# Performance work log

Measured on AMD Instinct MI355X. Metric: run time of the kernel, lower is better.

Reference implementation:

```python
import jax, jax.numpy as jnp
import numpy as np


def _segsum(x):
    """Stable segment-sum. x: (..., l) -> (..., l, l) lower-triangular sums."""
    l = x.shape[-1]
    cs = jnp.cumsum(x, axis=-1)
    seg = cs[..., :, None] - cs[..., None, :]
    mask = jnp.tril(jnp.ones((l, l), dtype=bool))
    return jnp.where(mask, seg, -jnp.inf)


def setup_inputs() -> dict:
    key = jax.random.key(0)
    kx, ka, kb, kc = jax.random.split(key, 4)
    b, s, h, p, n = 4, 8192, 32, 64, 16
    X = jax.random.normal(kx, (b, s, h, p), dtype=jnp.float32)
    # negative A for realistic decaying SSM dynamics / numerical safety
    A = -jnp.abs(jax.random.normal(ka, (b, s, h), dtype=jnp.float32)) * 0.5
    B = jax.random.normal(kb, (b, s, h, n), dtype=jnp.float32)
    C = jax.random.normal(kc, (b, s, h, n), dtype=jnp.float32)
    return {"X": X, "A": A, "B": B, "C": C, "block_len": 64}


def reference(X, A, B, C, block_len):
    b, s, h, p = X.shape
    n = B.shape[-1]
    c = s // block_len
    l = block_len
    # chunk: (b, c, l, ...)
    Xb = X.reshape(b, c, l, h, p)
    Bb = B.reshape(b, c, l, h, n)
    Cb = C.reshape(b, c, l, h, n)
    Ab = A.reshape(b, c, l, h).transpose(0, 3, 1, 2)  # (b, h, c, l)
    A_cumsum = jnp.cumsum(Ab, axis=-1)                # (b, h, c, l)

    # 1) intra-chunk (diagonal) output
    L = jnp.exp(_segsum(Ab))                          # (b, h, c, l, l)
    Y_diag = jnp.einsum("bclhn,bcshn,bhcls,bcshp->bclhp", Cb, Bb, L, Xb)

    # 2) intra-chunk states (chunk-final state contribution)
    decay_states = jnp.exp(A_cumsum[..., -1:] - A_cumsum)   # (b, h, c, l)
    states = jnp.einsum("bclhn,bhcl,bclhp->bchpn", Bb, decay_states, Xb)

    # 3) inter-chunk recurrence (zero initial states)
    A_last = A_cumsum[..., -1]                        # (b, h, c)
    decay_chunk = jnp.exp(_segsum(jnp.pad(A_last, ((0, 0), (0, 0), (1, 0)))))  # (b,h,c+1,c+1)
    states = jnp.concatenate([jnp.zeros_like(states[:, :1]), states], axis=1)  # (b,c+1,h,p,n)
    new_states = jnp.einsum("bhzc,bchpn->bzhpn", decay_chunk, states)
    states = new_states[:, :-1]                       # states entering each chunk

    # 4) state -> output (off-diagonal)
    state_decay_out = jnp.exp(A_cumsum)               # (b, h, c, l)
    Y_off = jnp.einsum("bclhn,bchpn,bhcl->bclhp", Cb, states, state_decay_out)

    Y = (Y_diag + Y_off).reshape(b, s, h, p)
    return Y
```

## Files before the change

kernel.cpp:

```cpp
#include <hip/hip_runtime.h>

#define BB 4
#define SS 8192
#define HH 32
#define PP 64
#define NN 16
#define LL 64
#define CC 128
#define NCHAIN (BB * HH)
#define NCHT (NCHAIN * CC)
#define ITERS 8
#define GRID1 (NCHT / ITERS)

typedef __attribute__((ext_vector_type(8))) short bf16x8;
typedef __attribute__((ext_vector_type(4))) short s16x4;
typedef __attribute__((ext_vector_type(4))) float f32x4;

#define LBAR() do { \
    __builtin_amdgcn_sched_barrier(0); \
    asm volatile("s_waitcnt lgkmcnt(0)" ::: "memory"); \
    __builtin_amdgcn_s_barrier(); \
    __builtin_amdgcn_sched_barrier(0); \
} while (0)

__device__ inline short f2bf(float f) {
    unsigned u = __builtin_bit_cast(unsigned, f);
    u = (u + 0x7FFFu + ((u >> 16) & 1u)) >> 16;
    return (short)u;
}
__device__ inline float bf2f(short s) {
    unsigned u = ((unsigned)(unsigned short)s) << 16;
    return __builtin_bit_cast(float, u);
}
__device__ inline float wscan(float v, int l) {
    float x = v;
#pragma unroll
    for (int d = 1; d < 64; d <<= 1) {
        float t = __shfl_up(x, d, 64);
        if (l >= d) x += t;
    }
    return x;
}

__global__ __launch_bounds__(256) void k1_states(
    const float* __restrict__ X, const float* __restrict__ A,
    const float* __restrict__ B, short* __restrict__ states,
    float* __restrict__ alast_g, short* __restrict__ xtf, int do_xtf)
{
    int tid = threadIdx.x;
    int w = tid >> 6, l = tid & 63, g = l >> 4, lr = l & 15;
    int r = tid >> 2, q4 = tid & 3;
    int bid = blockIdx.x;

    __shared__ float Bs[2][LL][17];

    float xrA[16], xrB[16];
    float4 br; float av;

#define K1_LOADS(gc_, xr_) { \
    int h_ = (gc_) & 31, c_ = ((gc_) >> 5) & 127, b_ = (gc_) >> 12; \
    size_t row0_ = (size_t)b_ * SS + (size_t)c_ * LL; \
    const float* Xp_ = X + (row0_ * HH + h_) * PP; \
    av = (A + row0_ * HH + h_)[(size_t)l * HH]; \
    br = *(const float4*)(B + (row0_ * HH + h_) * NN + (size_t)r * (HH * NN) + q4 * 4); \
    _Pragma("unroll") for (int kt_ = 0; kt_ < 2; ++kt_) \
    _Pragma("unroll") for (int e_ = 0; e_ < 8; ++e_) \
        xr_[kt_ * 8 + e_] = Xp_[(size_t)(kt_ * 32 + g * 8 + e_) * (HH * PP) + 16 * w + lr]; }

#define K1_STAGE(qd_, gc_) { \
    float x_ = wscan(av, l); \
    float alast_ = __shfl(x_, 63, 64); \
    float wlr_ = __expf(alast_ - __shfl(x_, r, 64)); \
    Bs[qd_][r][q4 * 4 + 0] = br.x * wlr_; \
    Bs[qd_][r][q4 * 4 + 1] = br.y * wlr_; \
    Bs[qd_][r][q4 * 4 + 2] = br.z * wlr_; \
    Bs[qd_][r][q4 * 4 + 3] = br.w * wlr_; \
    if (tid == 0) { \
        int h_ = (gc_) & 31, c_ = ((gc_) >> 5) & 127, b_ = (gc_) >> 12; \
        alast_g[(b_ * HH + h_) * CC + c_] = alast_; } }

#define K1_COMPUTE(qd_, xr_, gc_) { \
    int h_ = (gc_) & 31, c_ = ((gc_) >> 5) & 127, b_ = (gc_) >> 12; \
    size_t cc_ = (size_t)((b_ * HH + h_) * CC + c_); \
    bf16x8 bt0_, bt1_, xf0_, xf1_; \
    _Pragma("unroll") for (int e_ = 0; e_ < 8; ++e_) { \
        bt0_[e_] = f2bf(Bs[qd_][g * 8 + e_][lr]); \
        bt1_[e_] = f2bf(Bs[qd_][32 + g * 8 + e_][lr]); \
        xf0_[e_] = f2bf(xr_[e_]); xf1_[e_] = f2bf(xr_[8 + e_]); } \
    f32x4 st_ = __builtin_amdgcn_mfma_f32_16x16x32_bf16(bt0_, xf0_, (f32x4)0.f, 0, 0, 0); \
    st_ = __builtin_amdgcn_mfma_f32_16x16x32_bf16(bt1_, xf1_, st_, 0, 0, 0); \
    s16x4 sp_ = { f2bf(st_[0]), f2bf(st_[1]), f2bf(st_[2]), f2bf(st_[3]) }; \
    *(s16x4*)(states + (cc_ << 10) + ((16 * w + lr) << 4) + (g << 2)) = sp_; \
    if (do_xtf) { \
        short* xd_ = xtf + (cc_ << 12); \
        ((bf16x8*)xd_)[tid] = xf0_; \
        ((bf16x8*)xd_)[tid + 256] = xf1_; } }

    K1_LOADS(bid, xrA)
    K1_STAGE(0, bid)
    LBAR();
#pragma unroll
    for (int t = 0; t < ITERS; ++t) {
        int gc_c = bid + t * GRID1;
        int gc_n = bid + (t + 1) * GRID1;
        if (t + 1 < ITERS) {
            if (t & 1) { K1_LOADS(gc_n, xrA) } else { K1_LOADS(gc_n, xrB) }
        }
        if (t & 1) { K1_COMPUTE(t & 1, xrB, gc_c) } else { K1_COMPUTE(t & 1, xrA, gc_c) }
        if (t + 1 < ITERS) {
            K1_STAGE((t & 1) ^ 1, gc_n)
            LBAR();
        }
    }
#undef K1_LOADS
#undef K1_STAGE
#undef K1_COMPUTE
}

__global__ __launch_bounds__(256) void k2_scan(
    short* __restrict__ states, const float* __restrict__ alast_g)
{
    int chain = blockIdx.x >> 2;
    int t = ((blockIdx.x & 3) << 8) + threadIdx.x;
    __shared__ float eal[CC];
    if (threadIdx.x < CC)
        eal[threadIdx.x] = __expf(alast_g[chain * CC + threadIdx.x]);
    __syncthreads();

    short* base = states + ((size_t)chain * CC << 10) + t;
    float P = 0.f;
    for (int c0 = 0; c0 < CC; c0 += 8) {
        short s[8];
#pragma unroll
        for (int u = 0; u < 8; ++u) s[u] = base[(size_t)(c0 + u) << 10];
#pragma unroll
        for (int u = 0; u < 8; ++u) {
            float o = P;
            P = eal[c0 + u] * P + bf2f(s[u]);
            base[(size_t)(c0 + u) << 10] = f2bf(o);
        }
    }
}

__global__ __launch_bounds__(256) void k3_big(
    const float* __restrict__ A, const float* __restrict__ Bm,
    const float* __restrict__ Cm, const short* __restrict__ pin,
    const short* __restrict__ xtf, float* __restrict__ Y)
{
    int tid = threadIdx.x;
    int w = tid >> 6, l = tid & 63, g = l >> 4, lr = l & 15;
    int r = tid >> 2, q4 = tid & 3;
    int bid = blockIdx.x;

    __shared__ short ScF[8 * 64 * 8];
    __shared__ short BsF[2][4 * 64 * 8];
    __shared__ short CsF[2][4 * 64 * 8];
    __shared__ short PF [2][4 * 64 * 8];

    ((bf16x8*)ScF)[tid] = (bf16x8)0;
    ((bf16x8*)ScF)[tid + 256] = (bf16x8)0;
    if (tid < 128) {
        int zs = (tid >> 5) * 64 + 32 + (tid & 31);
        ((bf16x8*)BsF[0])[zs] = (bf16x8)0;  ((bf16x8*)BsF[1])[zs] = (bf16x8)0;
        ((bf16x8*)CsF[0])[zs] = (bf16x8)0;  ((bf16x8*)CsF[1])[zs] = (bf16x8)0;
        ((bf16x8*)PF [0])[zs] = (bf16x8)0;  ((bf16x8*)PF [1])[zs] = (bf16x8)0;
    }

    bf16x8 xv0n, xv1n, xv0c, xv1c;
    float4 br, cr0 = {0,0,0,0}, cr1 = {0,0,0,0};
    s16x4 pinb; float av;
    float x_c, x_n;

#define K3_LOADS(gc_) { \
    int h_ = (gc_) & 31, c_ = ((gc_) >> 5) & 127, b_ = (gc_) >> 12; \
    size_t row0_ = (size_t)b_ * SS + (size_t)c_ * LL; \
    size_t cc_ = (size_t)((b_ * HH + h_) * CC + c_); \
    const short* xs_ = xtf + (cc_ << 12); \
    xv0n = ((const bf16x8*)xs_)[tid]; \
    xv1n = ((const bf16x8*)xs_)[tid + 256]; \
    av = (A + row0_ * HH + h_)[(size_t)l * HH]; \
    br = *(const float4*)(Bm + (row0_ * HH + h_) * NN + (size_t)r * (HH * NN) + q4 * 4); \
    if (g < 2) { \
        const float* cp_ = Cm + (row0_ * HH + h_) * NN + (size_t)(16 * w + lr) * (HH * NN) + g * 8; \
        cr0 = *(const float4*)cp_; cr1 = *(const float4*)(cp_ + 4); } \
    pinb = *(const s16x4*)(pin + (cc_ << 10) + ((16 * w + lr) << 4) + (g << 2)); }

#define K3_STAGE(qd_) { \
    x_n = wscan(av, l); \
    int fl_ = (r & 15) + 16 * (q4 >> 1); \
    int jt_ = r >> 4; \
    s16x4 bb_ = { f2bf(br.x), f2bf(br.y), f2bf(br.z), f2bf(br.w) }; \
    ((s16x4*)BsF[qd_])[(jt_ * 64 + fl_) * 2 + (q4 & 1)] = bb_; \
    ((s16x4*)PF[qd_])[(w * 64 + (g >> 1) * 16 + lr) * 2 + (g & 1)] = pinb; \
    if (g < 2) { \
        bf16x8 cw_; \
        cw_[0]=f2bf(cr0.x); cw_[1]=f2bf(cr0.y); cw_[2]=f2bf(cr0.z); cw_[3]=f2bf(cr0.w); \
        cw_[4]=f2bf(cr1.x); cw_[5]=f2bf(cr1.y); cw_[6]=f2bf(cr1.z); cw_[7]=f2bf(cr1.w); \
        ((bf16x8*)CsF[qd_])[w * 64 + g * 16 + lr] = cw_; } }

#define SCORE_TILE(IT, JT, MASK) { \
    bf16x8 ca_ = ((bf16x8*)CsF[qb])[(IT) * 64 + l]; \
    bf16x8 bw_ = ((bf16x8*)BsF[qb])[(JT) * 64 + l]; \
    f32x4 sr_ = __builtin_amdgcn_mfma_f32_16x16x32_bf16(ca_, bw_, (f32x4)0.f, 0, 0, 0); \
    float csj_ = __shfl(x_c, (JT) * 16 + lr, 64); \
    float enj_ = __expf(-csj_); \
    _Pragma("unroll") for (int rr = 0; rr < 4; ++rr) { \
        float v_ = sr_[rr] * (eii[IT][rr] * enj_); \
        if (MASK) v_ = ((JT) * 16 + lr <= (IT) * 16 + 4 * g + rr) ? v_ : 0.f; \
        ScF[(((IT) * 2 + ((JT) >> 1)) * 64 + ((2 * (JT) + (lr >> 3)) & 3) * 16 + 4 * g + rr) * 8 + (lr & 7)] = f2bf(v_); } }

    K3_LOADS(bid)
    K3_STAGE(0)
    x_c = x_n; xv0c = xv0n; xv1c = xv1n;
    LBAR();

#pragma unroll 2
    for (int t = 0; t < ITERS; ++t) {
        int gc = bid + t * GRID1;
        int qb = t & 1;
        if (t + 1 < ITERS) { K3_LOADS(bid + (t + 1) * GRID1) }

        float eii[4][4];
#pragma unroll
        for (int it = 0; it < 4; ++it)
#pragma unroll
            for (int rr = 0; rr < 4; ++rr)
                eii[it][rr] = __expf(__shfl(x_c, 16 * it + 4 * g + rr, 64));

        f32x4 acc[4];
        {
            bf16x8 pfw = ((bf16x8*)PF[qb])[w * 64 + l];
#pragma unroll
            for (int it = 0; it < 4; ++it) {
                bf16x8 ca = ((bf16x8*)CsF[qb])[it * 64 + l];
                acc[it] = __builtin_amdgcn_mfma_f32_16x16x32_bf16(ca, pfw, (f32x4)0.f, 0, 0, 0);
            }
#pragma unroll
            for (int it = 0; it < 4; ++it)
#pragma unroll
                for (int rr = 0; rr < 4; ++rr) acc[it][rr] *= eii[it][rr];
        }

        if (w == 0)      { SCORE_TILE(0,0,true)  SCORE_TILE(2,1,false) SCORE_TILE(3,2,false) }
        else if (w == 1) { SCORE_TILE(1,0,false) SCORE_TILE(2,2,true)  SCORE_TILE(3,3,true)  }
        else if (w == 2) { SCORE_TILE(1,1,true)  SCORE_TILE(3,0,false) }
        else             { SCORE_TILE(2,0,false) SCORE_TILE(3,1,false) }

        LBAR();

#pragma unroll
        for (int it = 0; it < 4; ++it) {
            bf16x8 af0 = ((bf16x8*)ScF)[(it * 2 + 0) * 64 + l];
            acc[it] = __builtin_amdgcn_mfma_f32_16x16x32_bf16(af0, xv0c, acc[it], 0, 0, 0);
        }
#pragma unroll
        for (int it = 2; it < 4; ++it) {
            bf16x8 af1 = ((bf16x8*)ScF)[(it * 2 + 1) * 64 + l];
            acc[it] = __builtin_amdgcn_mfma_f32_16x16x32_bf16(af1, xv1c, acc[it], 0, 0, 0);
        }
        {
            int h_ = gc & 31, c_ = (gc >> 5) & 127, b_ = gc >> 12;
            size_t row0_ = (size_t)b_ * SS + (size_t)c_ * LL;
            float* Yp = Y + (row0_ * HH + h_) * PP;
#pragma unroll
            for (int it = 0; it < 4; ++it)
#pragma unroll
                for (int rr = 0; rr < 4; ++rr)
                    Yp[(size_t)(16 * it + 4 * g + rr) * (HH * PP) + 16 * w + lr] = acc[it][rr];
        }

        if (t + 1 < ITERS) { K3_STAGE((t + 1) & 1) }
        LBAR();
        x_c = x_n; xv0c = xv0n; xv1c = xv1n;
    }
#undef K3_LOADS
#undef K3_STAGE
#undef SCORE_TILE
}

__global__ __launch_bounds__(256) void k3_small(
    const float* __restrict__ X, const float* __restrict__ A,
    const float* __restrict__ Bm, const float* __restrict__ Cm,
    const short* __restrict__ pin, float* __restrict__ Y)
{
    int blk = blockIdx.x;
    int h = blk & (HH - 1);
    int c = (blk >> 5) & (CC - 1);
    int b = blk >> 12;
    int tid = threadIdx.x;
    int w = tid >> 6, l = tid & 63, g = l >> 4, lr = l & 15;
    int chain = b * HH + h;
    int r = tid >> 2, q = tid & 3;

    __shared__ short XTF[8 * 64 * 8];
    __shared__ short ScF[8 * 64 * 8];
    __shared__ short BsF[4 * 64 * 8];
    __shared__ short PF[4 * 64 * 8];

    size_t row0 = (size_t)b * SS + (size_t)c * LL;
    const float* Xp = X + (row0 * HH + h) * PP;
    const float* Bp = Bm + (row0 * HH + h) * NN;
    const float* Cp = Cm + (row0 * HH + h) * NN;
    const float* Ap = A + row0 * HH + h;
    float* Yp = Y + (row0 * HH + h) * PP;

    float av = Ap[(size_t)l * HH];
    float4 br = *(const float4*)(Bp + (size_t)r * (HH * NN) + q * 4);
    float4 cr0 = {0,0,0,0}, cr1 = {0,0,0,0};
    if (g < 2) {
        const float* crp = Cp + (size_t)(16 * w + lr) * (HH * NN) + g * 8;
        cr0 = *(const float4*)crp;
        cr1 = *(const float4*)(crp + 4);
    }
    s16x4 pinb = *(const s16x4*)(pin + (((size_t)(chain * CC + c)) << 10) + ((16 * w + lr) << 4) + (g << 2));
    float xr[16];
#pragma unroll
    for (int si = 0; si < 2; ++si)
#pragma unroll
        for (int e = 0; e < 8; ++e)
            xr[si * 8 + e] = Xp[(size_t)(si * 32 + g * 8 + e) * (HH * PP) + 16 * w + lr];

    float x = wscan(av, l);

    ((bf16x8*)ScF)[w * 128 + l] = (bf16x8)0;
    ((bf16x8*)ScF)[w * 128 + 64 + l] = (bf16x8)0;
    if (tid < 128)
        ((bf16x8*)PF)[(tid >> 5) * 64 + 32 + (tid & 31)] = (bf16x8)0;
    {
        int zt = tid >> 6, zu = (tid >> 1) & 31, zv = tid & 1;
        ((s16x4*)BsF)[(zt * 64 + 32 + zu) * 2 + zv] = (s16x4)0;
    }
    {
        int fl = (r & 15) + 16 * (q >> 1);
        int jt = r >> 4;
        s16x4 bb = { f2bf(br.x), f2bf(br.y), f2bf(br.z), f2bf(br.w) };
        ((s16x4*)BsF)[(jt * 64 + fl) * 2 + (q & 1)] = bb;
    }
    *(s16x4*)&PF[(w * 64 + (g >> 1) * 16 + lr) * 8 + (g & 1) * 4] = pinb;
    bf16x8 caw = (bf16x8)0;
    if (g < 2) {
        caw[0] = f2bf(cr0.x); caw[1] = f2bf(cr0.y);
        caw[2] = f2bf(cr0.z); caw[3] = f2bf(cr0.w);
        caw[4] = f2bf(cr1.x); caw[5] = f2bf(cr1.y);
        caw[6] = f2bf(cr1.z); caw[7] = f2bf(cr1.w);
    }
    __syncthreads();

    float cs_i[4], ei[4];
    int ib = 16 * w + 4 * g;
#pragma unroll
    for (int rr = 0; rr < 4; ++rr) {
        cs_i[rr] = __shfl(x, ib + rr, 64);
        ei[rr] = __expf(cs_i[rr]);
    }

    f32x4 acc[4];
#pragma unroll
    for (int pt = 0; pt < 4; ++pt) {
        bf16x8 pfv = ((bf16x8*)PF)[pt * 64 + l];
        acc[pt] = __builtin_amdgcn_mfma_f32_16x16x32_bf16(caw, pfv, (f32x4)0.f, 0, 0, 0);
    }
#pragma unroll
    for (int pt = 0; pt < 4; ++pt)
#pragma unroll
        for (int rr = 0; rr < 4; ++rr) acc[pt][rr] *= ei[rr];

    for (int jt = 0; jt <= w; ++jt) {
        bf16x8 bw = ((bf16x8*)BsF)[jt * 64 + l];
        f32x4 sr = __builtin_amdgcn_mfma_f32_16x16x32_bf16(caw, bw, (f32x4)0.f, 0, 0, 0);
        int j = jt * 16 + lr;
        float csj = __shfl(x, j, 64);
        int kt2 = j >> 5;
        int flb = 16 * ((j >> 3) & 3);
#pragma unroll
        for (int rr = 0; rr < 4; ++rr) {
            int i15 = g * 4 + rr;
            int i = 16 * w + i15;
            float v = (j <= i) ? sr[rr] * __expf(cs_i[rr] - csj) : 0.f;
            ScF[((w * 2 + kt2) * 64 + i15 + flb) * 8 + (j & 7)] = f2bf(v);
        }
    }

#pragma unroll
    for (int si = 0; si < 2; ++si) {
        bf16x8 xb;
#pragma unroll
        for (int e = 0; e < 8; ++e) xb[e] = f2bf(xr[si * 8 + e]);
        ((bf16x8*)XTF)[tid + si * 256] = xb;
    }
    __syncthreads();

    int kts = (w >= 2) ? 2 : 1;
    for (int kt = 0; kt < kts; ++kt) {
        bf16x8 af = ((bf16x8*)ScF)[(w * 2 + kt) * 64 + l];
#pragma unroll
        for (int pt = 0; pt < 4; ++pt) {
            bf16x8 xf = ((bf16x8*)XTF)[(kt * 4 + pt) * 64 + l];
            acc[pt] = __builtin_amdgcn_mfma_f32_16x16x32_bf16(af, xf, acc[pt], 0, 0, 0);
        }
    }

#pragma unroll
    for (int pt = 0; pt < 4; ++pt)
#pragma unroll
        for (int rr = 0; rr < 4; ++rr)
            Yp[(size_t)(16 * w + 4 * g + rr) * (HH * PP) + pt * 16 + lr] = acc[pt][rr];
}

extern "C" void kernel_launch(void* const* d_in, const int* in_sizes, int n_in,
                              void* d_out, int out_size, void* d_ws, size_t ws_size,
                              hipStream_t stream)
{
    const float* X = (const float*)d_in[0];
    const float* A = (const float*)d_in[1];
    const float* B = (const float*)d_in[2];
    const float* C = (const float*)d_in[3];
    float* Y = (float*)d_out;

    const size_t states_bytes = (size_t)NCHT * 1024 * 2;
    const size_t alast_bytes  = (size_t)NCHT * 4;
    const size_t xtf_bytes    = (size_t)NCHT * 4096 * 2;
    short* states = (short*)d_ws;
    float* alast  = (float*)((char*)d_ws + states_bytes);
    short* xtf    = (short*)((char*)d_ws + states_bytes + alast_bytes);
    int big = (ws_size >= states_bytes + alast_bytes + xtf_bytes) ? 1 : 0;

    dim3 blk(256);
    k1_states<<<dim3(GRID1), blk, 0, stream>>>(X, A, B, states, alast, xtf, big);
    k2_scan<<<dim3(NCHAIN * 4), blk, 0, stream>>>(states, alast);
    if (big)
        k3_big<<<dim3(GRID1), blk, 0, stream>>>(A, B, C, states, xtf, Y);
    else
        k3_small<<<dim3(NCHT), blk, 0, stream>>>(X, A, B, C, states, Y);
}
```

Before: 257.6 us.

## Vectorize scan to paired bf16, coalesce C loads, hoist exps, add setprio

The scan kernel now handles two bf16 state elements per thread via 32-bit accesses and launches half as many blocks. In k3, C is loaded by every thread with the same coalesced float4 pattern as B, replacing the half-wave 8-wide loads. Exponentials are computed once per lane and broadcast by shuffle instead of being recomputed per tile, and s_setprio is raised around the MFMA sections. The cost is less parallelism in the scan and a changed C LDS layout that must still match the SCORE_TILE reads.

```diff
diff --git a/kernel.cpp b/kernel.cpp
--- a/kernel.cpp
+++ b/kernel.cpp
@@ -120,24 +120,29 @@
 __global__ __launch_bounds__(256) void k2_scan(
     short* __restrict__ states, const float* __restrict__ alast_g)
 {
-    int chain = blockIdx.x >> 2;
-    int t = ((blockIdx.x & 3) << 8) + threadIdx.x;
+    int chain = blockIdx.x >> 1;
+    int t2 = ((blockIdx.x & 1) << 8) + threadIdx.x;
     __shared__ float eal[CC];
     if (threadIdx.x < CC)
         eal[threadIdx.x] = __expf(alast_g[chain * CC + threadIdx.x]);
     __syncthreads();
 
-    short* base = states + ((size_t)chain * CC << 10) + t;
-    float P = 0.f;
+    unsigned* base = (unsigned*)(states + ((size_t)chain * CC << 10)) + t2;
+    float P0 = 0.f, P1 = 0.f;
     for (int c0 = 0; c0 < CC; c0 += 8) {
-        short s[8];
-#pragma unroll
-        for (int u = 0; u < 8; ++u) s[u] = base[(size_t)(c0 + u) << 10];
+        unsigned s[8];
+#pragma unroll
+        for (int u = 0; u < 8; ++u) s[u] = base[(size_t)(c0 + u) << 9];
 #pragma unroll
         for (int u = 0; u < 8; ++u) {
-            float o = P;
-            P = eal[c0 + u] * P + bf2f(s[u]);
-            base[(size_t)(c0 + u) << 10] = f2bf(o);
+            float e = eal[c0 + u];
+            float f0 = bf2f((short)(s[u] & 0xFFFFu));
+            float f1 = bf2f((short)(s[u] >> 16));
+            unsigned o = (unsigned)(unsigned short)f2bf(P0)
+                       | ((unsigned)(unsigned short)f2bf(P1) << 16);
+            P0 = e * P0 + f0;
+            P1 = e * P1 + f1;
+            base[(size_t)(c0 + u) << 9] = o;
         }
     }
 }
@@ -167,7 +172,7 @@
     }
 
     bf16x8 xv0n, xv1n, xv0c, xv1c;
-    float4 br, cr0 = {0,0,0,0}, cr1 = {0,0,0,0};
+    float4 br, crv;
     s16x4 pinb; float av;
     float x_c, x_n;
 
@@ -180,9 +185,7 @@
     xv1n = ((const bf16x8*)xs_)[tid + 256]; \
     av = (A + row0_ * HH + h_)[(size_t)l * HH]; \
     br = *(const float4*)(Bm + (row0_ * HH + h_) * NN + (size_t)r * (HH * NN) + q4 * 4); \
-    if (g < 2) { \
-        const float* cp_ = Cm + (row0_ * HH + h_) * NN + (size_t)(16 * w + lr) * (HH * NN) + g * 8; \
-        cr0 = *(const float4*)cp_; cr1 = *(const float4*)(cp_ + 4); } \
+    crv = *(const float4*)(Cm + (row0_ * HH + h_) * NN + (size_t)r * (HH * NN) + q4 * 4); \
     pinb = *(const s16x4*)(pin + (cc_ << 10) + ((16 * w + lr) << 4) + (g << 2)); }
 
 #define K3_STAGE(qd_) { \
@@ -191,19 +194,15 @@
     int jt_ = r >> 4; \
     s16x4 bb_ = { f2bf(br.x), f2bf(br.y), f2bf(br.z), f2bf(br.w) }; \
     ((s16x4*)BsF[qd_])[(jt_ * 64 + fl_) * 2 + (q4 & 1)] = bb_; \
-    ((s16x4*)PF[qd_])[(w * 64 + (g >> 1) * 16 + lr) * 2 + (g & 1)] = pinb; \
-    if (g < 2) { \
-        bf16x8 cw_; \
-        cw_[0]=f2bf(cr0.x); cw_[1]=f2bf(cr0.y); cw_[2]=f2bf(cr0.z); cw_[3]=f2bf(cr0.w); \
-        cw_[4]=f2bf(cr1.x); cw_[5]=f2bf(cr1.y); cw_[6]=f2bf(cr1.z); cw_[7]=f2bf(cr1.w); \
-        ((bf16x8*)CsF[qd_])[w * 64 + g * 16 + lr] = cw_; } }
+    s16x4 cc_ = { f2bf(crv.x), f2bf(crv.y), f2bf(crv.z), f2bf(crv.w) }; \
+    ((s16x4*)CsF[qd_])[(jt_ * 64 + fl_) * 2 + (q4 & 1)] = cc_; \
+    ((s16x4*)PF[qd_])[(w * 64 + (g >> 1) * 16 + lr) * 2 + (g & 1)] = pinb; }
 
 #define SCORE_TILE(IT, JT, MASK) { \
     bf16x8 ca_ = ((bf16x8*)CsF[qb])[(IT) * 64 + l]; \
     bf16x8 bw_ = ((bf16x8*)BsF[qb])[(JT) * 64 + l]; \
     f32x4 sr_ = __builtin_amdgcn_mfma_f32_16x16x32_bf16(ca_, bw_, (f32x4)0.f, 0, 0, 0); \
-    float csj_ = __shfl(x_c, (JT) * 16 + lr, 64); \
-    float enj_ = __expf(-csj_); \
+    float enj_ = __shfl(en_l, (JT) * 16 + lr, 64); \
     _Pragma("unroll") for (int rr = 0; rr < 4; ++rr) { \
         float v_ = sr_[rr] * (eii[IT][rr] * enj_); \
         if (MASK) v_ = ((JT) * 16 + lr <= (IT) * 16 + 4 * g + rr) ? v_ : 0.f; \
@@ -220,13 +219,16 @@
         int qb = t & 1;
         if (t + 1 < ITERS) { K3_LOADS(bid + (t + 1) * GRID1) }
 
+        float ei_l = __expf(x_c);
+        float en_l = __expf(-x_c);
         float eii[4][4];
 #pragma unroll
         for (int it = 0; it < 4; ++it)
 #pragma unroll
             for (int rr = 0; rr < 4; ++rr)
-                eii[it][rr] = __expf(__shfl(x_c, 16 * it + 4 * g + rr, 64));
-
+                eii[it][rr] = __shfl(ei_l, 16 * it + 4 * g + rr, 64);
+
+        __builtin_amdgcn_s_setprio(1);
         f32x4 acc[4];
         {
             bf16x8 pfw = ((bf16x8*)PF[qb])[w * 64 + l];
@@ -245,9 +247,11 @@
         else if (w == 1) { SCORE_TILE(1,0,false) SCORE_TILE(2,2,true)  SCORE_TILE(3,3,true)  }
         else if (w == 2) { SCORE_TILE(1,1,true)  SCORE_TILE(3,0,false) }
         else             { SCORE_TILE(2,0,false) SCORE_TILE(3,1,false) }
+        __builtin_amdgcn_s_setprio(0);
 
         LBAR();
 
+        __builtin_amdgcn_s_setprio(1);
 #pragma unroll
         for (int it = 0; it < 4; ++it) {
             bf16x8 af0 = ((bf16x8*)ScF)[(it * 2 + 0) * 64 + l];
@@ -258,6 +262,7 @@
             bf16x8 af1 = ((bf16x8*)ScF)[(it * 2 + 1) * 64 + l];
             acc[it] = __builtin_amdgcn_mfma_f32_16x16x32_bf16(af1, xv1c, acc[it], 0, 0, 0);
         }
+        __builtin_amdgcn_s_setprio(0);
         {
             int h_ = gc & 31, c_ = (gc >> 5) & 127, b_ = gc >> 12;
             size_t row0_ = (size_t)b_ * SS + (size_t)c_ * LL;
@@ -427,7 +432,7 @@
 
     dim3 blk(256);
     k1_states<<<dim3(GRID1), blk, 0, stream>>>(X, A, B, states, alast, xtf, big);
-    k2_scan<<<dim3(NCHAIN * 4), blk, 0, stream>>>(states, alast);
+    k2_scan<<<dim3(NCHAIN * 2), blk, 0, stream>>>(states, alast);
     if (big)
         k3_big<<<dim3(GRID1), blk, 0, stream>>>(A, B, C, states, xtf, Y);
     else
```

After: 252.3 us. 1.02x faster.
